# Kernel optimization log

Measured on AMD Instinct MI355X. Metric: run time of the kernel, lower is better.

## Reference

```python
import jax, jax.numpy as jnp
import numpy as np

N, C, T, V, D = 64, 64, 256, 25, 64
BN_EPS = 1e-5


def _make_shift(v, ch, sign):
    idx = np.empty(v * ch, dtype=np.int64)
    for i in range(v):
        for j in range(ch):
            idx[i * ch + j] = (i * ch + j + sign * j * ch) % (ch * v)
    return jnp.asarray(idx, dtype=jnp.int32)


def setup_inputs() -> dict:
    key = jax.random.key(0)
    ks = jax.random.split(key, 8)
    return {
        "x0": jax.random.normal(ks[0], (N, C, T, V), dtype=jnp.float32),
        "fc1_w": jax.random.normal(ks[1], (C // 4, C), dtype=jnp.float32) * (1.0 / np.sqrt(C)),
        "fc1_b": jnp.zeros((C // 4,), dtype=jnp.float32),
        "fc2_w": jax.random.normal(ks[2], (4, C // 4), dtype=jnp.float32) * (1.0 / np.sqrt(C // 4)),
        "fc2_b": jnp.zeros((4,), dtype=jnp.float32),
        "Linear_weight": jax.random.normal(ks[3], (4, C, D), dtype=jnp.float32) * np.sqrt(1.0 / D),
        "Linear_bias": jax.random.normal(ks[4], (4, D), dtype=jnp.float32) * 0.02,
        "Feature_Mask": jax.random.normal(ks[5], (1, V, C), dtype=jnp.float32) * 0.1,
        "bn_gamma": 1.0 + 0.05 * jax.random.normal(ks[6], (V * D,), dtype=jnp.float32),
        "bn_beta": 0.05 * jax.random.normal(ks[7], (V * D,), dtype=jnp.float32),
        "shift_in": _make_shift(V, C, +1),
        "shift_out": _make_shift(V, D, -1),
        "epoch": 100,
    }


def reference(x0, fc1_w, fc1_b, fc2_w, fc2_b, Linear_weight, Linear_bias,
              Feature_Mask, bn_gamma, bn_beta, shift_in, shift_out, epoch):
    n, c, t, v = x0.shape
    d = Linear_weight.shape[-1]

    # DY_SEModule gate: global avg pool -> 1x1 convs -> tempered softmax over 4
    pooled = x0.mean(axis=(2, 3))                       # [n, c]
    h = jax.nn.relu(pooled @ fc1_w.T + fc1_b)           # [n, c//4]
    logits = h @ fc2_w.T + fc2_b                        # [n, 4]
    tao = (-(30.0 - 1.0) / 60.0 * epoch + 30.0) if epoch < 60 else 1.0
    gate = jax.nn.softmax(logits / tao, axis=1)         # [n, 4]

    # per-sample fused weights / bias
    W_fuse = jnp.einsum('kcd,nk->ncd', Linear_weight, gate)   # [n, c, d]
    b_fuse = jnp.einsum('kc,nk->nc', Linear_bias, gate)       # [n, d]

    # shift-in gather over flattened (v*c) channel axis
    x = x0.transpose(0, 2, 3, 1).reshape(n * t, v * c)  # [n*t, v*c]
    x = x[:, shift_in].reshape(n * t, v, c)
    x = x * (jnp.tanh(Feature_Mask) + 1.0)              # learnable feature mask
    x = x.reshape(n, t, v, c)

    # per-sample dynamic linear + bias
    x = jnp.einsum('ntvc,ncd->ntvd', x, W_fuse) + b_fuse[:, None, None, :]

    # shift-out gather
    x = x.reshape(n * t, v * d)[:, shift_out]           # [n*t, v*d]

    # BatchNorm1d (training mode: batch statistics over n*t)
    mean = x.mean(axis=0)
    var = jnp.var(x, axis=0)
    x = (x - mean) * jax.lax.rsqrt(var + BN_EPS) * bn_gamma + bn_beta

    x = x.reshape(n, t, v, d).transpose(0, 3, 1, 2)     # [n, d, t, v]
    return jax.nn.relu(x + x0)                          # identity residual (c == d)
```

## Files before the change

kernel.cpp:

```cpp
#include <hip/hip_runtime.h>
#include <hip/hip_bf16.h>
#include <math.h>

#define NN 64
#define CC 64
#define TT 256
#define VV 25
#define DD 64
#define BN_EPS 1e-5f
#define NREP 16

typedef short bf16x8 __attribute__((ext_vector_type(8)));
typedef float f32x4 __attribute__((ext_vector_type(4)));

#define WS_POOLED 0
#define WS_GATE   4096
#define WS_BFUSE  4352
#define WS_MASK   8448
#define WS_ABP    10048
#define WS_S1     13248
#define WS_S2     38848
#define WS_WTB    64448
#define WS_YB     195520

static __device__ __forceinline__ unsigned short f2bf(float x) {
    __hip_bfloat16 h = __float2bfloat16(x);
    return *(unsigned short*)&h;
}
static __device__ __forceinline__ float bf2f(unsigned short u) {
    return __uint_as_float(((unsigned)u) << 16);
}
static __device__ __forceinline__ void gload_lds16(const void* gsrc, void* ldst) {
    typedef const __attribute__((address_space(1))) unsigned int gu32;
    typedef __attribute__((address_space(3))) unsigned int lu32;
    __builtin_amdgcn_global_load_lds((gu32*)gsrc, (lu32*)ldst, 16, 0, 0);
}

__global__ __launch_bounds__(256) void k_mask(const float* __restrict__ fmask, float* ws) {
    const int f = blockIdx.x * 256 + threadIdx.x;
    if (f < VV * CC) ws[WS_MASK + f] = tanhf(fmask[f]) + 1.0f;
}

__global__ __launch_bounds__(256) void k_xt(const float* __restrict__ x0,
                                            const float* __restrict__ ws,
                                            float* __restrict__ pooled,
                                            unsigned short* __restrict__ xT) {
    __shared__ __align__(16) float tile[64][104];
    const int n = blockIdx.y, tcb = blockIdx.x;
    const int tid = threadIdx.x;
    const size_t nbase = (size_t)n * (CC * TT * VV);
    const int col0 = tcb * 100;

    for (int l4 = tid; l4 < 1600; l4 += 256) {
        const int c = l4 / 25, q = l4 - c * 25;
        const float4 v = *(const float4*)(x0 + nbase + c * 6400 + col0 + 4 * q);
        *(float4*)&tile[c][4 * q] = v;
    }
    __syncthreads();

    if (tid < 64) {
        float s = 0.f;
        for (int q = 0; q < 25; q++) {
            const float4 v = *(const float4*)&tile[tid][4 * q];
            s += v.x + v.y + v.z + v.w;
        }
        atomicAdd(&pooled[n * 64 + tid], s * (1.f / 6400.f));
    }

    const float* maskg = ws + WS_MASK;
    for (int l = tid; l < 800; l += 256) {
        const int row = l >> 3;
        const int jb = (l & 7) * 8;
        const int trel = row / 25, i = row - trel * 25;
        const float4 m0 = *(const float4*)(maskg + i * 64 + jb);
        const float4 m1 = *(const float4*)(maskg + i * 64 + jb + 4);
        const float mk[8] = {m0.x, m0.y, m0.z, m0.w, m1.x, m1.y, m1.z, m1.w};
        unsigned outw[4];
#pragma unroll
        for (int pair = 0; pair < 4; pair++) {
            unsigned lo = 0, hi = 0;
#pragma unroll
            for (int hl = 0; hl < 2; hl++) {
                const int j = jb + pair * 2 + hl;
                int jm = j; if (jm >= 50) jm -= 50; else if (jm >= 25) jm -= 25;
                int p = i + jm; if (p >= 25) p -= 25;
                const float v = tile[j][trel * 25 + p] * mk[pair * 2 + hl];
                if (hl == 0) lo = (unsigned)f2bf(v); else hi = (unsigned)f2bf(v);
            }
            outw[pair] = lo | (hi << 16);
        }
        const int grow = col0 + row;
        const int jswz = ((l & 7) ^ (grow & 7)) * 8;
        *(uint4*)(xT + ((size_t)(n * 6400) + grow) * 64 + jswz) = *(uint4*)outw;
    }
}

__global__ __launch_bounds__(256) void k_gate(const float* __restrict__ fc1_w,
                                              const float* __restrict__ fc1_b,
                                              const float* __restrict__ fc2_w,
                                              const float* __restrict__ fc2_b,
                                              const float* __restrict__ lin_b,
                                              const int* __restrict__ epoch_p,
                                              float* ws) {
    const int tid = threadIdx.x;
    float* pooled = ws + WS_POOLED;
    float* gate   = ws + WS_GATE;
    float* bfuse  = ws + WS_BFUSE;

    if (tid < 64) {
        const int n = tid;
        const float* po = pooled + n * 64;
        float h[16];
        for (int q = 0; q < 16; q++) {
            float z = fc1_b[q];
            for (int j = 0; j < 64; j++) z = fmaf(fc1_w[q * 64 + j], po[j], z);
            h[q] = fmaxf(z, 0.f);
        }
        float lg[4];
        for (int k = 0; k < 4; k++) {
            float z = fc2_b[k];
            for (int q = 0; q < 16; q++) z = fmaf(fc2_w[k * 16 + q], h[q], z);
            lg[k] = z;
        }
        const int ep = epoch_p[0];
        const float tao = (ep < 60) ? (-(29.0f / 60.0f) * (float)ep + 30.0f) : 1.0f;
        float mx = -1e30f;
        for (int k = 0; k < 4; k++) { lg[k] /= tao; mx = fmaxf(mx, lg[k]); }
        float se = 0.f;
        for (int k = 0; k < 4; k++) { lg[k] = expf(lg[k] - mx); se += lg[k]; }
        const float inv = 1.f / se;
        for (int k = 0; k < 4; k++) gate[n * 4 + k] = lg[k] * inv;
    }
    __syncthreads();
    for (int f = tid; f < 4096; f += 256) {
        const int n = f >> 6, d = f & 63;
        float s = 0.f;
        for (int k = 0; k < 4; k++) s = fmaf(lin_b[k * 64 + d], gate[n * 4 + k], s);
        bfuse[f] = s;
    }
}

__global__ __launch_bounds__(256) void k_wfuse(const float* __restrict__ lw, float* ws) {
    __shared__ float tile[64 * 65];
    const float* gate = ws + WS_GATE;
    unsigned short* wtb = (unsigned short*)(ws + WS_WTB);
    const int n = blockIdx.x;
    float g[4];
    for (int k = 0; k < 4; k++) g[k] = gate[n * 4 + k];
    for (int f = threadIdx.x; f < 4096; f += 256) {
        const int c = f >> 6, d = f & 63;
        float v = g[0] * lw[f] + g[1] * lw[4096 + f] + g[2] * lw[8192 + f] + g[3] * lw[12288 + f];
        tile[d * 65 + c] = v;
    }
    __syncthreads();
    for (int f = threadIdx.x; f < 4096; f += 256) {
        const int d = f >> 6, c = f & 63;
        wtb[n * 4096 + f] = f2bf(tile[d * 65 + c]);
    }
}

__global__ __launch_bounds__(256, 4) void k_gemm(const unsigned short* __restrict__ xT,
                                                 const unsigned short* __restrict__ wtb,
                                                 const float* __restrict__ ws,
                                                 float* __restrict__ wsmut) {
    __shared__ __align__(16) char pool[36352];
    unsigned short (*Wl)[72] = (unsigned short(*)[72])(pool);
    unsigned short* Xm = (unsigned short*)(pool + 9216);
    unsigned short* outl = (unsigned short*)(pool + 23552);

    const int n = blockIdx.y, tb = blockIdx.x;
    const int tid = threadIdx.x;
    const int wv = tid >> 6, lane = tid & 63;
    const int lrow = lane & 15, lgrp = lane >> 4;
    const int dcol = wv * 16 + lrow;

    {
        const uint4* wsrc = (const uint4*)(wtb + n * 4096);
#pragma unroll
        for (int it = 0; it < 2; it++) {
            const int itx = tid + it * 256;
            uint4 u = wsrc[itx];
            const int f8 = itx * 8;
            *(uint4*)&Wl[f8 >> 6][f8 & 63] = u;
        }
    }
    const float bfv = ws[WS_BFUSE + n * 64 + dcol];

    {
        const char* xc = (const char*)(xT + ((size_t)n * 6400 + tb * 400) * 64);
#pragma unroll
        for (int it = 0; it < 4; it++) {
            const int off = it * 4096 + tid * 16;
            if (off < 14336) gload_lds16(xc + off, (char*)Xm + off);
        }
    }
    __syncthreads();
    const bf16x8 w0 = *(const bf16x8*)&Wl[dcol][8 * lgrp];
    const bf16x8 w1 = *(const bf16x8*)&Wl[dcol][32 + 8 * lgrp];

    float s1r[7][4], s2r[7][4];
#pragma unroll
    for (int m = 0; m < 7; m++)
#pragma unroll
        for (int r = 0; r < 4; r++) { s1r[m][r] = 0.f; s2r[m][r] = 0.f; }

    unsigned short* yg = (unsigned short*)(wsmut + WS_YB) + (size_t)n * 64 * 6400;

    for (int ck = 0; ck < 4; ck++) {
        const int rowt = tb * 400 + ck * 100;
        asm volatile("s_waitcnt vmcnt(0)" ::: "memory");
        __syncthreads();

        const int b7 = rowt & 7;
#pragma unroll
        for (int m = 0; m < 7; m++) {
            const int rloc = m * 16 + lrow;
            const int r7 = (rloc + b7) & 7;
            const bf16x8 a0 = *(const bf16x8*)(Xm + rloc * 64 + ((lgrp ^ r7) << 3));
            const bf16x8 a1 = *(const bf16x8*)(Xm + rloc * 64 + (((lgrp + 4) ^ r7) << 3));
            f32x4 a = {bfv, bfv, bfv, bfv};
            a = __builtin_amdgcn_mfma_f32_16x16x32_bf16(a0, w0, a, 0, 0, 0);
            a = __builtin_amdgcn_mfma_f32_16x16x32_bf16(a1, w1, a, 0, 0, 0);
#pragma unroll
            for (int r = 0; r < 4; r++) {
                const int row = m * 16 + 4 * lgrp + r;
                if (row < 100) {
                    const unsigned short us = f2bf(a[r]);
                    const float yf = bf2f(us);
                    s1r[m][r] += yf;
                    s2r[m][r] = fmaf(yf, yf, s2r[m][r]);
                    outl[dcol * 100 + row] = us;
                }
            }
        }
        __syncthreads();

        if (ck < 3) {
            const char* xc = (const char*)(xT + ((size_t)n * 6400 + rowt + 100) * 64);
#pragma unroll
            for (int it = 0; it < 4; it++) {
                const int off = it * 4096 + tid * 16;
                if (off < 14336) gload_lds16(xc + off, (char*)Xm + off);
            }
        }
        for (int l = tid; l < 1600; l += 256) {
            const int dd = l / 25, q = l - dd * 25;
            const uint2 u = *(const uint2*)(outl + dd * 100 + 4 * q);
            *(uint2*)(yg + (size_t)dd * 6400 + rowt + 4 * q) = u;
        }
    }

    float* s1l = (float*)Xm;
    float* s2l = s1l + 1650;
    for (int f = tid; f < 3300; f += 256) s1l[f] = 0.f;
    __syncthreads();
#pragma unroll
    for (int m = 0; m < 7; m++) {
#pragma unroll
        for (int r = 0; r < 4; r++) {
            const int row = m * 16 + 4 * lgrp + r;
            if (row < 100) {
                int v = row;
                if (v >= 75) v -= 75; else if (v >= 50) v -= 50; else if (v >= 25) v -= 25;
                __hip_atomic_fetch_add(&s1l[v * 66 + dcol], s1r[m][r],
                                       __ATOMIC_RELAXED, __HIP_MEMORY_SCOPE_WORKGROUP);
                __hip_atomic_fetch_add(&s2l[v * 66 + dcol], s2r[m][r],
                                       __ATOMIC_RELAXED, __HIP_MEMORY_SCOPE_WORKGROUP);
            }
        }
    }
    __syncthreads();
    const int rep = (n * 5 + tb) & (NREP - 1);
    float* g1 = wsmut + WS_S1 + rep * 1600;
    float* g2 = wsmut + WS_S2 + rep * 1600;
    for (int f = tid; f < 1600; f += 256) {
        atomicAdd(&g1[f], s1l[(f >> 6) * 66 + (f & 63)]);
        atomicAdd(&g2[f], s2l[(f >> 6) * 66 + (f & 63)]);
    }
}

__global__ __launch_bounds__(256) void k_finalize(const float* __restrict__ gamma,
                                                  const float* __restrict__ beta,
                                                  float* ws) {
    const int f = blockIdx.x * 256 + threadIdx.x;
    if (f >= VV * DD) return;
    const int v = f >> 6, d = f & 63;
    const int vi = (v - d + 175) % 25;
    const int fin = vi * 64 + d;
    float s1 = 0.f, s2 = 0.f;
    for (int rep = 0; rep < NREP; rep++) {
        s1 += ws[WS_S1 + rep * 1600 + fin];
        s2 += ws[WS_S2 + rep * 1600 + fin];
    }
    const float mean = s1 * (1.f / (NN * TT));
    float var = s2 * (1.f / (NN * TT)) - mean * mean;
    var = fmaxf(var, 0.f);
    const float rs = rsqrtf(var + BN_EPS);
    const float a = gamma[f] * rs;
    const float b = beta[f] - mean * a;
    ((unsigned*)ws)[WS_ABP + f] = (unsigned)f2bf(a) | (((unsigned)f2bf(b)) << 16);
}

__global__ __launch_bounds__(256) void k_bn(const float* __restrict__ x0,
                                            const float* __restrict__ ws,
                                            float* __restrict__ out) {
    __shared__ __align__(16) unsigned short ybL[6400];
    __shared__ float aL[25], bL[25];
    const int d = blockIdx.x, n = blockIdx.y;
    const int tid = threadIdx.x;
    const size_t pbase = (size_t)(n * 64 + d) * 6400;
    const unsigned short* yb = (const unsigned short*)(ws + WS_YB);

    for (int l = tid; l < 800; l += 256)
        *(uint4*)&ybL[l * 8] = *(const uint4*)(yb + pbase + l * 8);
    if (tid < 25) {
        const unsigned u = ((const unsigned*)ws)[WS_ABP + tid * 64 + d];
        aL[tid] = __uint_as_float(u << 16);
        bL[tid] = __uint_as_float(u & 0xffff0000u);
    }
    __syncthreads();

    const int sh = d % 25;
    for (int l4 = tid; l4 < 1600; l4 += 256) {
        const int e0 = 4 * l4;
        const float4 xv = *(const float4*)(x0 + pbase + e0);
        int t = e0 / 25;
        int vo = e0 - 25 * t;
        float o[4];
        const float xe[4] = {xv.x, xv.y, xv.z, xv.w};
#pragma unroll
        for (int k = 0; k < 4; k++) {
            int vs = vo - sh; if (vs < 0) vs += 25;
            const float y = bf2f(ybL[t * 25 + vs]);
            o[k] = fmaxf(fmaf(aL[vo], y, bL[vo]) + xe[k], 0.f);
            vo++; if (vo >= 25) { vo = 0; t++; }
        }
        float4 ov = {o[0], o[1], o[2], o[3]};
        *(float4*)(out + pbase + e0) = ov;
    }
}

extern "C" void kernel_launch(void* const* d_in, const int* in_sizes, int n_in,
                              void* d_out, int out_size, void* d_ws, size_t ws_size,
                              hipStream_t stream) {
    const float* x0    = (const float*)d_in[0];
    const float* fc1_w = (const float*)d_in[1];
    const float* fc1_b = (const float*)d_in[2];
    const float* fc2_w = (const float*)d_in[3];
    const float* fc2_b = (const float*)d_in[4];
    const float* lw    = (const float*)d_in[5];
    const float* lb    = (const float*)d_in[6];
    const float* fmask = (const float*)d_in[7];
    const float* gamma = (const float*)d_in[8];
    const float* beta  = (const float*)d_in[9];
    const int* epoch   = (const int*)d_in[12];
    float* ws  = (float*)d_ws;
    float* out = (float*)d_out;
    unsigned short* xT = (unsigned short*)d_out;
    const unsigned short* wtb = (const unsigned short*)(ws + WS_WTB);

    hipMemsetAsync(d_ws, 0, (size_t)WS_WTB * sizeof(float), stream);

    k_mask<<<7, 256, 0, stream>>>(fmask, ws);
    k_xt<<<dim3(64, 64), 256, 0, stream>>>(x0, ws, ws + WS_POOLED, xT);
    k_gate<<<1, 256, 0, stream>>>(fc1_w, fc1_b, fc2_w, fc2_b, lb, epoch, ws);
    k_wfuse<<<NN, 256, 0, stream>>>(lw, ws);
    k_gemm<<<dim3(16, 64), 256, 0, stream>>>(xT, wtb, ws, ws);
    k_finalize<<<7, 256, 0, stream>>>(gamma, beta, ws);
    k_bn<<<dim3(64, 64), 256, 0, stream>>>(x0, ws, out);
}
```

Measured before the change: 211.7 us.

## Store GEMM output row-major and retile GEMM/BN over 128-row and 100-column chunks

The GEMM kernel now launches 50 tiles of 128 rows per sample, each loaded once instead of four pipelined 100-row chunks. It writes y in row-major (t,v)×d order straight to global memory, with no LDS transpose staging. BN statistics are accumulated with per-element LDS atomics instead of register partials. The BN kernel is retiled so each block covers 100 columns across all 64 channels, reading the row-major y and the full a/b table through padded LDS. The intent is to drop the LDS transpose and loop sync overhead and raise GEMM parallelism. In exchange it adds many LDS atomics and scattered 2-byte global stores.

```diff
diff --git a/kernel.cpp b/kernel.cpp
--- a/kernel.cpp
+++ b/kernel.cpp
@@ -163,17 +163,25 @@
                                                  const unsigned short* __restrict__ wtb,
                                                  const float* __restrict__ ws,
                                                  float* __restrict__ wsmut) {
-    __shared__ __align__(16) char pool[36352];
+    __shared__ __align__(16) char pool[38800];
     unsigned short (*Wl)[72] = (unsigned short(*)[72])(pool);
     unsigned short* Xm = (unsigned short*)(pool + 9216);
-    unsigned short* outl = (unsigned short*)(pool + 23552);
+    float* s1l = (float*)(pool + 25600);
+    float* s2l = (float*)(pool + 32200);
 
     const int n = blockIdx.y, tb = blockIdx.x;
+    const int rowbase = tb * 128;
     const int tid = threadIdx.x;
     const int wv = tid >> 6, lane = tid & 63;
     const int lrow = lane & 15, lgrp = lane >> 4;
     const int dcol = wv * 16 + lrow;
 
+    {
+        const char* xc = (const char*)(xT + ((size_t)n * 6400 + rowbase) * 64);
+#pragma unroll
+        for (int it = 0; it < 4; it++)
+            gload_lds16(xc + it * 4096 + tid * 16, (char*)Xm + it * 4096 + tid * 16);
+    }
     {
         const uint4* wsrc = (const uint4*)(wtb + n * 4096);
 #pragma unroll
@@ -183,94 +191,43 @@
             const int f8 = itx * 8;
             *(uint4*)&Wl[f8 >> 6][f8 & 63] = u;
         }
+        for (int f = tid; f < 3300; f += 256) s1l[f] = 0.f;
     }
     const float bfv = ws[WS_BFUSE + n * 64 + dcol];
-
-    {
-        const char* xc = (const char*)(xT + ((size_t)n * 6400 + tb * 400) * 64);
-#pragma unroll
-        for (int it = 0; it < 4; it++) {
-            const int off = it * 4096 + tid * 16;
-            if (off < 14336) gload_lds16(xc + off, (char*)Xm + off);
-        }
-    }
-    __syncthreads();
+    __syncthreads();
+
     const bf16x8 w0 = *(const bf16x8*)&Wl[dcol][8 * lgrp];
     const bf16x8 w1 = *(const bf16x8*)&Wl[dcol][32 + 8 * lgrp];
 
-    float s1r[7][4], s2r[7][4];
-#pragma unroll
-    for (int m = 0; m < 7; m++)
-#pragma unroll
-        for (int r = 0; r < 4; r++) { s1r[m][r] = 0.f; s2r[m][r] = 0.f; }
-
-    unsigned short* yg = (unsigned short*)(wsmut + WS_YB) + (size_t)n * 64 * 6400;
-
-    for (int ck = 0; ck < 4; ck++) {
-        const int rowt = tb * 400 + ck * 100;
-        asm volatile("s_waitcnt vmcnt(0)" ::: "memory");
-        __syncthreads();
-
-        const int b7 = rowt & 7;
-#pragma unroll
-        for (int m = 0; m < 7; m++) {
-            const int rloc = m * 16 + lrow;
-            const int r7 = (rloc + b7) & 7;
-            const bf16x8 a0 = *(const bf16x8*)(Xm + rloc * 64 + ((lgrp ^ r7) << 3));
-            const bf16x8 a1 = *(const bf16x8*)(Xm + rloc * 64 + (((lgrp + 4) ^ r7) << 3));
-            f32x4 a = {bfv, bfv, bfv, bfv};
-            a = __builtin_amdgcn_mfma_f32_16x16x32_bf16(a0, w0, a, 0, 0, 0);
-            a = __builtin_amdgcn_mfma_f32_16x16x32_bf16(a1, w1, a, 0, 0, 0);
-#pragma unroll
-            for (int r = 0; r < 4; r++) {
-                const int row = m * 16 + 4 * lgrp + r;
-                if (row < 100) {
-                    const unsigned short us = f2bf(a[r]);
-                    const float yf = bf2f(us);
-                    s1r[m][r] += yf;
-                    s2r[m][r] = fmaf(yf, yf, s2r[m][r]);
-                    outl[dcol * 100 + row] = us;
-                }
-            }
-        }
-        __syncthreads();
-
-        if (ck < 3) {
-            const char* xc = (const char*)(xT + ((size_t)n * 6400 + rowt + 100) * 64);
-#pragma unroll
-            for (int it = 0; it < 4; it++) {
-                const int off = it * 4096 + tid * 16;
-                if (off < 14336) gload_lds16(xc + off, (char*)Xm + off);
-            }
-        }
-        for (int l = tid; l < 1600; l += 256) {
-            const int dd = l / 25, q = l - dd * 25;
-            const uint2 u = *(const uint2*)(outl + dd * 100 + 4 * q);
-            *(uint2*)(yg + (size_t)dd * 6400 + rowt + 4 * q) = u;
-        }
-    }
-
-    float* s1l = (float*)Xm;
-    float* s2l = s1l + 1650;
-    for (int f = tid; f < 3300; f += 256) s1l[f] = 0.f;
-    __syncthreads();
-#pragma unroll
-    for (int m = 0; m < 7; m++) {
+    unsigned short* yg = (unsigned short*)(wsmut + WS_YB) + ((size_t)n * 6400 + rowbase) * 64;
+    const int vbase = rowbase % 25;
+    const int r7 = lrow & 7;
+
+#pragma unroll
+    for (int m = 0; m < 8; m++) {
+        const int rloc = m * 16 + lrow;
+        const bf16x8 a0 = *(const bf16x8*)(Xm + rloc * 64 + ((lgrp ^ r7) << 3));
+        const bf16x8 a1 = *(const bf16x8*)(Xm + rloc * 64 + (((lgrp + 4) ^ r7) << 3));
+        f32x4 a = {bfv, bfv, bfv, bfv};
+        a = __builtin_amdgcn_mfma_f32_16x16x32_bf16(a0, w0, a, 0, 0, 0);
+        a = __builtin_amdgcn_mfma_f32_16x16x32_bf16(a1, w1, a, 0, 0, 0);
 #pragma unroll
         for (int r = 0; r < 4; r++) {
             const int row = m * 16 + 4 * lgrp + r;
-            if (row < 100) {
-                int v = row;
-                if (v >= 75) v -= 75; else if (v >= 50) v -= 50; else if (v >= 25) v -= 25;
-                __hip_atomic_fetch_add(&s1l[v * 66 + dcol], s1r[m][r],
-                                       __ATOMIC_RELAXED, __HIP_MEMORY_SCOPE_WORKGROUP);
-                __hip_atomic_fetch_add(&s2l[v * 66 + dcol], s2r[m][r],
-                                       __ATOMIC_RELAXED, __HIP_MEMORY_SCOPE_WORKGROUP);
-            }
-        }
-    }
-    __syncthreads();
-    const int rep = (n * 5 + tb) & (NREP - 1);
+            const unsigned short us = f2bf(a[r]);
+            const float yf = bf2f(us);
+            int vv = vbase + row;
+            vv -= (vv >= 125) ? 125 : (vv >= 100) ? 100 : (vv >= 75) ? 75 :
+                  (vv >= 50) ? 50 : (vv >= 25) ? 25 : 0;
+            __hip_atomic_fetch_add(&s1l[vv * 66 + dcol], yf,
+                                   __ATOMIC_RELAXED, __HIP_MEMORY_SCOPE_WORKGROUP);
+            __hip_atomic_fetch_add(&s2l[vv * 66 + dcol], yf * yf,
+                                   __ATOMIC_RELAXED, __HIP_MEMORY_SCOPE_WORKGROUP);
+            yg[(size_t)row * 64 + dcol] = us;
+        }
+    }
+    __syncthreads();
+    const int rep = (n * 50 + tb) & (NREP - 1);
     float* g1 = wsmut + WS_S1 + rep * 1600;
     float* g2 = wsmut + WS_S2 + rep * 1600;
     for (int f = tid; f < 1600; f += 256) {
@@ -304,39 +261,44 @@
 __global__ __launch_bounds__(256) void k_bn(const float* __restrict__ x0,
                                             const float* __restrict__ ws,
                                             float* __restrict__ out) {
-    __shared__ __align__(16) unsigned short ybL[6400];
-    __shared__ float aL[25], bL[25];
-    const int d = blockIdx.x, n = blockIdx.y;
+    __shared__ __align__(16) unsigned short yL[100 * 68];
+    __shared__ unsigned ABl[25 * 68];
+    const int tcb = blockIdx.x, n = blockIdx.y;
     const int tid = threadIdx.x;
-    const size_t pbase = (size_t)(n * 64 + d) * 6400;
-    const unsigned short* yb = (const unsigned short*)(ws + WS_YB);
-
-    for (int l = tid; l < 800; l += 256)
-        *(uint4*)&ybL[l * 8] = *(const uint4*)(yb + pbase + l * 8);
-    if (tid < 25) {
-        const unsigned u = ((const unsigned*)ws)[WS_ABP + tid * 64 + d];
-        aL[tid] = __uint_as_float(u << 16);
-        bL[tid] = __uint_as_float(u & 0xffff0000u);
-    }
-    __syncthreads();
-
-    const int sh = d % 25;
+    const int col0 = tcb * 100;
+    const unsigned short* yg = (const unsigned short*)(ws + WS_YB) + ((size_t)n * 6400 + col0) * 64;
+
+    for (int g = tid; g < 1600; g += 256) {
+        const uint2 u = *(const uint2*)(yg + g * 4);
+        *(uint2*)&yL[(g >> 4) * 68 + (g & 15) * 4] = u;
+    }
+    const unsigned* abp = (const unsigned*)(ws + WS_ABP);
+    for (int f = tid; f < 1600; f += 256)
+        ABl[(f >> 6) * 68 + (f & 63)] = abp[f];
+    __syncthreads();
+
+    const size_t pbase = (size_t)n * (CC * TT * VV);
     for (int l4 = tid; l4 < 1600; l4 += 256) {
-        const int e0 = 4 * l4;
-        const float4 xv = *(const float4*)(x0 + pbase + e0);
-        int t = e0 / 25;
-        int vo = e0 - 25 * t;
+        const int dd = l4 / 25, q = l4 - dd * 25;
+        const int c0 = 4 * q;
+        const float4 xv = *(const float4*)(x0 + pbase + dd * 6400 + col0 + c0);
+        const int sh = dd - ((dd >= 50) ? 50 : (dd >= 25) ? 25 : 0);
         float o[4];
         const float xe[4] = {xv.x, xv.y, xv.z, xv.w};
 #pragma unroll
         for (int k = 0; k < 4; k++) {
+            const int col = c0 + k;
+            const int tl = (col >= 75) ? 3 : (col >= 50) ? 2 : (col >= 25) ? 1 : 0;
+            const int vo = col - tl * 25;
             int vs = vo - sh; if (vs < 0) vs += 25;
-            const float y = bf2f(ybL[t * 25 + vs]);
-            o[k] = fmaxf(fmaf(aL[vo], y, bL[vo]) + xe[k], 0.f);
-            vo++; if (vo >= 25) { vo = 0; t++; }
+            const unsigned u = ABl[vo * 68 + dd];
+            const float a_ = __uint_as_float(u << 16);
+            const float b_ = __uint_as_float(u & 0xffff0000u);
+            const float y = bf2f(yL[(tl * 25 + vs) * 68 + dd]);
+            o[k] = fmaxf(fmaf(a_, y, b_) + xe[k], 0.f);
         }
         float4 ov = {o[0], o[1], o[2], o[3]};
-        *(float4*)(out + pbase + e0) = ov;
+        *(float4*)(out + pbase + dd * 6400 + col0 + c0) = ov;
     }
 }
 
@@ -365,7 +327,7 @@
     k_xt<<<dim3(64, 64), 256, 0, stream>>>(x0, ws, ws + WS_POOLED, xT);
     k_gate<<<1, 256, 0, stream>>>(fc1_w, fc1_b, fc2_w, fc2_b, lb, epoch, ws);
     k_wfuse<<<NN, 256, 0, stream>>>(lw, ws);
-    k_gemm<<<dim3(16, 64), 256, 0, stream>>>(xT, wtb, ws, ws);
+    k_gemm<<<dim3(50, 64), 256, 0, stream>>>(xT, wtb, ws, ws);
     k_finalize<<<7, 256, 0, stream>>>(gamma, beta, ws);
     k_bn<<<dim3(64, 64), 256, 0, stream>>>(x0, ws, out);
 }
```

Measured after the change: 412.2 us. +94.7%, slower.

## Double-buffer X tiles in LDS and use per-wave output staging in GEMM

Applied to the files above, without the earlier changes.

The GEMM kernel now double-buffers the X chunk loads in two LDS buffers, issuing prefetches two chunks ahead with vmcnt-based waits. This replaces the single buffer that forced a full wait and barrier each chunk. The fused weights are loaded straight from global memory into registers, skipping the LDS staging. Each wave writes its own output slice to a private LDS region, so the barrier between the MFMA work and the global stores goes away. In exchange, LDS use rises and the occupancy hint of 4 blocks is dropped, and correctness now depends on hand-tuned vmcnt counts.

```diff
diff --git a/kernel.cpp b/kernel.cpp
--- a/kernel.cpp
+++ b/kernel.cpp
@@ -159,44 +159,40 @@
     }
 }
 
-__global__ __launch_bounds__(256, 4) void k_gemm(const unsigned short* __restrict__ xT,
-                                                 const unsigned short* __restrict__ wtb,
-                                                 const float* __restrict__ ws,
-                                                 float* __restrict__ wsmut) {
-    __shared__ __align__(16) char pool[36352];
-    unsigned short (*Wl)[72] = (unsigned short(*)[72])(pool);
-    unsigned short* Xm = (unsigned short*)(pool + 9216);
-    unsigned short* outl = (unsigned short*)(pool + 23552);
-
+__global__ __launch_bounds__(256) void k_gemm(const unsigned short* __restrict__ xT,
+                                              const unsigned short* __restrict__ wtb,
+                                              const float* __restrict__ ws,
+                                              float* __restrict__ wsmut) {
+    __shared__ __align__(16) char pool[45568];
     const int n = blockIdx.y, tb = blockIdx.x;
     const int tid = threadIdx.x;
     const int wv = tid >> 6, lane = tid & 63;
     const int lrow = lane & 15, lgrp = lane >> 4;
     const int dcol = wv * 16 + lrow;
 
+    unsigned short* outw = (unsigned short*)(pool + 32768) + wv * 1600;
+
+    const bf16x8 w0 = *(const bf16x8*)(wtb + n * 4096 + dcol * 64 + 8 * lgrp);
+    const bf16x8 w1 = *(const bf16x8*)(wtb + n * 4096 + dcol * 64 + 32 + 8 * lgrp);
+    const float bfv = ws[WS_BFUSE + n * 64 + dcol];
+    asm volatile("" ::: "memory");
+
+    const char* xbase = (const char*)(xT + (size_t)n * 6400 * 64);
     {
-        const uint4* wsrc = (const uint4*)(wtb + n * 4096);
-#pragma unroll
-        for (int it = 0; it < 2; it++) {
-            const int itx = tid + it * 256;
-            uint4 u = wsrc[itx];
-            const int f8 = itx * 8;
-            *(uint4*)&Wl[f8 >> 6][f8 & 63] = u;
-        }
-    }
-    const float bfv = ws[WS_BFUSE + n * 64 + dcol];
-
+        const char* src = xbase + (size_t)(tb * 400) * 128;
+#pragma unroll
+        for (int it = 0; it < 4; it++)
+            gload_lds16(src + it * 4096 + tid * 16, pool + it * 4096 + tid * 16);
+    }
+    asm volatile("" ::: "memory");
     {
-        const char* xc = (const char*)(xT + ((size_t)n * 6400 + tb * 400) * 64);
-#pragma unroll
-        for (int it = 0; it < 4; it++) {
-            const int off = it * 4096 + tid * 16;
-            if (off < 14336) gload_lds16(xc + off, (char*)Xm + off);
-        }
-    }
-    __syncthreads();
-    const bf16x8 w0 = *(const bf16x8*)&Wl[dcol][8 * lgrp];
-    const bf16x8 w1 = *(const bf16x8*)&Wl[dcol][32 + 8 * lgrp];
+        const char* src = xbase + (size_t)(tb * 400 + 100) * 128;
+#pragma unroll
+        for (int it = 0; it < 4; it++)
+            gload_lds16(src + it * 4096 + tid * 16, pool + 16384 + it * 4096 + tid * 16);
+    }
+    asm volatile("s_waitcnt vmcnt(4)" ::: "memory");
+    asm volatile("s_barrier" ::: "memory");
 
     float s1r[7][4], s2r[7][4];
 #pragma unroll
@@ -206,12 +202,12 @@
 
     unsigned short* yg = (unsigned short*)(wsmut + WS_YB) + (size_t)n * 64 * 6400;
 
+#pragma unroll
     for (int ck = 0; ck < 4; ck++) {
         const int rowt = tb * 400 + ck * 100;
-        asm volatile("s_waitcnt vmcnt(0)" ::: "memory");
-        __syncthreads();
-
-        const int b7 = rowt & 7;
+        const unsigned short* Xm = (const unsigned short*)(pool + (ck & 1) * 16384);
+        const int b7 = (ck & 1) * 4;
+
 #pragma unroll
         for (int m = 0; m < 7; m++) {
             const int rloc = m * 16 + lrow;
@@ -229,28 +225,34 @@
                     const float yf = bf2f(us);
                     s1r[m][r] += yf;
                     s2r[m][r] = fmaf(yf, yf, s2r[m][r]);
-                    outl[dcol * 100 + row] = us;
+                    outw[lrow * 100 + row] = us;
                 }
             }
         }
-        __syncthreads();
-
+#pragma unroll
+        for (int it = 0; it < 7; it++) {
+            const int l = lane + it * 64;
+            if (l < 400) {
+                const int dloc = l / 25, q = l - dloc * 25;
+                const uint2 u = *(const uint2*)(outw + dloc * 100 + 4 * q);
+                *(uint2*)(yg + (size_t)(wv * 16 + dloc) * 6400 + rowt + 4 * q) = u;
+            }
+        }
         if (ck < 3) {
-            const char* xc = (const char*)(xT + ((size_t)n * 6400 + rowt + 100) * 64);
-#pragma unroll
-            for (int it = 0; it < 4; it++) {
-                const int off = it * 4096 + tid * 16;
-                if (off < 14336) gload_lds16(xc + off, (char*)Xm + off);
-            }
-        }
-        for (int l = tid; l < 1600; l += 256) {
-            const int dd = l / 25, q = l - dd * 25;
-            const uint2 u = *(const uint2*)(outl + dd * 100 + 4 * q);
-            *(uint2*)(yg + (size_t)dd * 6400 + rowt + 4 * q) = u;
-        }
-    }
-
-    float* s1l = (float*)Xm;
+            asm volatile("s_waitcnt vmcnt(7)" ::: "memory");
+            asm volatile("s_barrier" ::: "memory");
+            if (ck < 2) {
+                const char* src = xbase + (size_t)(tb * 400 + (ck + 2) * 100) * 128;
+                char* dst = pool + (ck & 1) * 16384;
+#pragma unroll
+                for (int it = 0; it < 4; it++)
+                    gload_lds16(src + it * 4096 + tid * 16, dst + it * 4096 + tid * 16);
+            }
+        }
+    }
+
+    __syncthreads();
+    float* s1l = (float*)pool;
     float* s2l = s1l + 1650;
     for (int f = tid; f < 3300; f += 256) s1l[f] = 0.f;
     __syncthreads();
@@ -260,11 +262,11 @@
         for (int r = 0; r < 4; r++) {
             const int row = m * 16 + 4 * lgrp + r;
             if (row < 100) {
-                int v = row;
-                if (v >= 75) v -= 75; else if (v >= 50) v -= 50; else if (v >= 25) v -= 25;
-                __hip_atomic_fetch_add(&s1l[v * 66 + dcol], s1r[m][r],
+                int vv = row;
+                if (vv >= 75) vv -= 75; else if (vv >= 50) vv -= 50; else if (vv >= 25) vv -= 25;
+                __hip_atomic_fetch_add(&s1l[vv * 66 + dcol], s1r[m][r],
                                        __ATOMIC_RELAXED, __HIP_MEMORY_SCOPE_WORKGROUP);
-                __hip_atomic_fetch_add(&s2l[v * 66 + dcol], s2r[m][r],
+                __hip_atomic_fetch_add(&s2l[vv * 66 + dcol], s2r[m][r],
                                        __ATOMIC_RELAXED, __HIP_MEMORY_SCOPE_WORKGROUP);
             }
         }
```

Measured after the change: 211.5 us. About the same (-0.1%).
